# Kernel tuning notes

Measured on AMD Instinct MI355X. Metric: run time of the kernel, lower is better.

Reference implementation:

```python
import jax, jax.numpy as jnp
import numpy as np
from jax import lax

D_MODEL = 1024
D_STATE = 16
D_CONV = 4
EXPAND = 2
D_INNER = EXPAND * D_MODEL
DT_RANK = (D_MODEL + 15) // 16  # ceil(d_model/16) = 64
B, L = 2, 2048
EPS = 1e-5


def setup_inputs() -> dict:
    key = jax.random.key(0)
    ks = jax.random.split(key, 12)
    s = 0.02
    inp = {
        "x": jax.random.normal(ks[0], (B, L, D_MODEL), jnp.float32),
        "ln_g": jnp.ones((D_MODEL,), jnp.float32),
        "ln_b": jnp.zeros((D_MODEL,), jnp.float32),
        "sq_w": jax.random.normal(ks[1], (D_MODEL, D_MODEL), jnp.float32) * s,
        "sq_b": jnp.zeros((D_MODEL,), jnp.float32),
        "srw_w": jax.random.normal(ks[2], (D_MODEL, D_MODEL), jnp.float32) * s,
        "srw_b": jnp.zeros((D_MODEL,), jnp.float32),
        "res_scale": jnp.ones((1,), jnp.float32),
        "in_proj_w": jax.random.normal(ks[3], (D_MODEL, 2 * D_INNER), jnp.float32) * s,
        "conv_w": jax.random.normal(ks[4], (D_INNER, D_CONV), jnp.float32) * 0.1,
        "conv_b": jnp.zeros((D_INNER,), jnp.float32),
        "x_proj_w": jax.random.normal(ks[5], (D_INNER, DT_RANK + 2 * D_STATE), jnp.float32) * s,
        "dt_w": jax.random.normal(ks[6], (DT_RANK, D_INNER), jnp.float32) * s,
        "dt_b": jnp.full((D_INNER,), -4.6, jnp.float32),  # softplus(-4.6)~0.01
        "A_log": jnp.log(jnp.broadcast_to(jnp.arange(1, D_STATE + 1, dtype=jnp.float32), (D_INNER, D_STATE))),
        "D": jnp.ones((D_INNER,), jnp.float32),
        "out_proj_w": jax.random.normal(ks[7], (D_INNER, D_MODEL), jnp.float32) * s,
    }
    return inp


def _layernorm(x, g, b):
    mu = jnp.mean(x, axis=-1, keepdims=True)
    var = jnp.mean(jnp.square(x - mu), axis=-1, keepdims=True)
    return (x - mu) * lax.rsqrt(var + EPS) * g + b


def _causal_dwconv(u, w, b):
    # u: [B,L,Din], w: [Din,d_conv] -> causal depthwise conv
    din, dc = w.shape
    up = jnp.pad(u, ((0, 0), (dc - 1, 0), (0, 0)))
    k = w.T[:, None, :]  # [d_conv, 1, Din]
    out = lax.conv_general_dilated(up, k, (1,), "VALID",
                                   dimension_numbers=("NWC", "WIO", "NWC"),
                                   feature_group_count=din)
    return out + b


def _mamba(h, in_proj_w, conv_w, conv_b, x_proj_w, dt_w, dt_b, A_log, D, out_proj_w):
    xz = h @ in_proj_w                       # [B,L,2*Din]
    u, z = jnp.split(xz, 2, axis=-1)
    u = jax.nn.silu(_causal_dwconv(u, conv_w, conv_b))  # [B,L,Din]
    x_dbl = u @ x_proj_w                     # [B,L,R+2N]
    dt, Bm, Cm = jnp.split(x_dbl, [DT_RANK, DT_RANK + D_STATE], axis=-1)
    delta = jax.nn.softplus(dt @ dt_w + dt_b)            # [B,L,Din]
    A = -jnp.exp(A_log)                                  # [Din,N]
    dA = jnp.exp(jnp.einsum("bld,dn->bldn", delta, A))   # [B,L,Din,N]
    dBu = jnp.einsum("bld,bln,bld->bldn", delta, Bm, u)  # [B,L,Din,N]

    def step(hst, inp):
        dA_t, dBu_t, C_t = inp
        hst = dA_t * hst + dBu_t                         # [B,Din,N]
        y = jnp.einsum("bdn,bn->bd", hst, C_t)
        return hst, y

    h0 = jnp.zeros((u.shape[0], D_INNER, D_STATE), u.dtype)
    _, ys = lax.scan(step, h0, (dA.transpose(1, 0, 2, 3),
                                dBu.transpose(1, 0, 2, 3),
                                Cm.transpose(1, 0, 2)))
    y = ys.transpose(1, 0, 2) + u * D                    # [B,L,Din]
    y = y * jax.nn.silu(z)
    return y @ out_proj_w


def reference(x, ln_g, ln_b, sq_w, sq_b, srw_w, srw_b, res_scale,
              in_proj_w, conv_w, conv_b, x_proj_w, dt_w, dt_b, A_log, D, out_proj_w):
    residual = x
    h = _layernorm(x, ln_g, ln_b)
    h = h + (h @ sq_w + sq_b)                # x + spatial_query(x)
    y = _mamba(h, in_proj_w, conv_w, conv_b, x_proj_w, dt_w, dt_b, A_log, D, out_proj_w)
    y = y * (y @ srw_w + srw_b)              # x * spatial_reweight(x)
    return residual + res_scale * y
```

## Files before the change

kernel.cpp:

```cpp
#include <hip/hip_runtime.h>
#include <math.h>


#define DMODEL 1024
#define DINNER 2048
#define NSTATE 16
#define DTRANK 64
#define BATCH  2
#define SEQ    2048
#define ROWS   (BATCH*SEQ)
#define NC     32
#define TS     (SEQ/NC)
#define LN_EPS 1e-5f

typedef unsigned short u16;
typedef __attribute__((ext_vector_type(8))) short bf16x8;
typedef __attribute__((ext_vector_type(4))) float f32x4;

__device__ __forceinline__ float silu_f(float x) { return x / (1.f + __expf(-x)); }

__device__ __forceinline__ u16 f2bf(float f) {
    union { float f; unsigned u; } v; v.f = f;
    unsigned r = v.u + 0x7fffu + ((v.u >> 16) & 1u);
    return (u16)(r >> 16);
}
__device__ __forceinline__ float bf2f(u16 h) {
    union { unsigned u; float f; } v; v.u = ((unsigned)h) << 16; return v.f;
}

__device__ __forceinline__ void gload_lds16(const u16* g, u16* l) {
    __builtin_amdgcn_global_load_lds(
        (const __attribute__((address_space(1))) unsigned int*)(g),
        (__attribute__((address_space(3))) unsigned int*)(static_cast<void*>(l)),
        16, 0, 0);
}

__device__ __forceinline__ void tr_tile(const float* __restrict__ src,
                                        u16* __restrict__ dst,
                                        int R, int C, int xt, int yt, int tx, int ty)
{
    __shared__ float t[32][33];
    int c0 = xt * 32, r0 = yt * 32;
    #pragma unroll
    for (int i = 0; i < 32; i += 8) {
        float v = 0.f;
        if (c0 + tx < C) v = src[(size_t)(r0 + ty + i) * C + c0 + tx];
        t[ty + i][tx] = v;
    }
    __syncthreads();
    #pragma unroll
    for (int i = 0; i < 32; i += 8)
        dst[(size_t)(c0 + ty + i) * R + r0 + tx] = f2bf(t[tx][ty + i]);
}

__global__ __launch_bounds__(256) void prologue_kernel(
    const float* __restrict__ sq_w,  u16* __restrict__ sqT,
    const float* __restrict__ srw_w, u16* __restrict__ srwT,
    const float* __restrict__ inp,   u16* __restrict__ inpT,
    const float* __restrict__ outp,  u16* __restrict__ outpT,
    const float* __restrict__ xp,    u16* __restrict__ xpT,
    const float* __restrict__ dtw,   u16* __restrict__ dtT,
    const float* __restrict__ x,     const float* __restrict__ ln_g,
    const float* __restrict__ ln_b,
    float* __restrict__ h0, u16* __restrict__ h0bf)
{
    int id = blockIdx.x;
    if (id < 8576) {
        int tx = threadIdx.x & 31, ty = threadIdx.x >> 5;
        if (id < 1024)      { tr_tile(sq_w,  sqT,  1024, 1024, id & 31,  id >> 5, tx, ty); }
        else if (id < 2048) { id -= 1024; tr_tile(srw_w, srwT, 1024, 1024, id & 31,  id >> 5, tx, ty); }
        else if (id < 6144) { id -= 2048; tr_tile(inp,  inpT, 1024, 4096, id & 127, id >> 7, tx, ty); }
        else if (id < 8192) { id -= 6144; tr_tile(outp, outpT,2048, 1024, id & 31,  id >> 5, tx, ty); }
        else if (id < 8448) { id -= 8192; tr_tile(xp,   xpT,  2048,   96, id & 3,   id >> 2, tx, ty); }
        else                { id -= 8448; tr_tile(dtw,  dtT,    64, 2048, id & 63,  id >> 6, tx, ty); }
        return;
    }
    int row = id - 8576;
    const float* xr = x + (size_t)row * DMODEL;
    float4 v = ((const float4*)xr)[threadIdx.x];
    float s  = v.x + v.y + v.z + v.w;
    float ss = v.x*v.x + v.y*v.y + v.z*v.z + v.w*v.w;
    #pragma unroll
    for (int off = 32; off; off >>= 1) { s += __shfl_down(s, off); ss += __shfl_down(ss, off); }
    __shared__ float s_s[4], s_ss[4];
    int lane = threadIdx.x & 63, w = threadIdx.x >> 6;
    if (lane == 0) { s_s[w] = s; s_ss[w] = ss; }
    __syncthreads();
    float ts = 0.f, tss = 0.f;
    #pragma unroll
    for (int i = 0; i < 4; i++) { ts += s_s[i]; tss += s_ss[i]; }
    float mu  = ts / (float)DMODEL;
    float var = tss / (float)DMODEL - mu * mu;
    float rstd = rsqrtf(var + LN_EPS);
    float4 gv = ((const float4*)ln_g)[threadIdx.x];
    float4 bv = ((const float4*)ln_b)[threadIdx.x];
    float4 o;
    o.x = (v.x - mu) * rstd * gv.x + bv.x;
    o.y = (v.y - mu) * rstd * gv.y + bv.y;
    o.z = (v.z - mu) * rstd * gv.z + bv.z;
    o.w = (v.w - mu) * rstd * gv.w + bv.w;
    ((float4*)(h0 + (size_t)row * DMODEL))[threadIdx.x] = o;
    unsigned lo = (unsigned)f2bf(o.x) | ((unsigned)f2bf(o.y) << 16);
    unsigned hi = (unsigned)f2bf(o.z) | ((unsigned)f2bf(o.w) << 16);
    ((uint2*)(h0bf + (size_t)row * DMODEL))[threadIdx.x] = make_uint2(lo, hi);
}

__device__ __forceinline__ void stage128(const u16* __restrict__ A, const u16* __restrict__ Bt,
                                         int m0, int n0, int lda, int ldb, int k0,
                                         u16* As, u16* Bs, int tid)
{
    #pragma unroll
    for (int p = 0; p < 2; p++) {
        int idx = p * 256 + tid;
        int row = idx >> 2, seg = idx & 3;
        int ss = seg ^ ((row >> 1) & 3);
        gload_lds16(A  + (size_t)(m0 + row) * lda + k0 + ss * 8, As + idx * 8);
        gload_lds16(Bt + (size_t)(n0 + row) * ldb + k0 + ss * 8, Bs + idx * 8);
    }
}
__device__ __forceinline__ void stage256(const u16* __restrict__ A, const u16* __restrict__ Bt,
                                         int m0, int n0, int lda, int ldb, int k0,
                                         u16* As, u16* Bs, int tid)
{
    #pragma unroll
    for (int p = 0; p < 2; p++) {
        int idx = p * 512 + tid;
        int row = idx >> 2, seg = idx & 3;
        int ss = seg ^ ((row >> 1) & 3);
        gload_lds16(A  + (size_t)(m0 + row) * lda + k0 + ss * 8, As + idx * 8);
        gload_lds16(Bt + (size_t)(n0 + row) * ldb + k0 + ss * 8, Bs + idx * 8);
    }
}

__device__ __forceinline__ void ph128(int t, int nt,
    const u16* __restrict__ A, const u16* __restrict__ Bt,
    int m0, int n0, int lda, int ldb, int tid, int wr, int wc, int g, int r,
    u16* As, u16* Bs, bf16x8 (&avR)[4], bf16x8 (&avW)[4], f32x4 (&acc)[4][4])
{
    if (t + 1 < nt) {
        asm volatile("s_waitcnt vmcnt(0)" ::: "memory");
        __builtin_amdgcn_s_barrier();
        __builtin_amdgcn_sched_barrier(0);
    }
    bf16x8 bv[4];
    {
        const u16* bc = Bs + (t % 3) * 4096;
        #pragma unroll
        for (int ni = 0; ni < 4; ni++) {
            int brow = wc * 64 + ni * 16 + r;
            bv[ni] = *(const bf16x8*)&bc[brow * 32 + ((g ^ ((brow >> 1) & 3)) << 3)];
        }
    }
    __builtin_amdgcn_sched_barrier(0);
    if (t + 1 < nt) {
        const u16* ac = As + ((t + 1) % 3) * 4096;
        #pragma unroll
        for (int mi = 0; mi < 4; mi++) {
            int arow = wr * 64 + mi * 16 + r;
            avW[mi] = *(const bf16x8*)&ac[arow * 32 + ((g ^ ((arow >> 1) & 3)) << 3)];
        }
    }
    if (t + 2 < nt)
        stage128(A, Bt, m0, n0, lda, ldb, (t + 2) << 5,
                 As + ((t + 2) % 3) * 4096, Bs + ((t + 2) % 3) * 4096, tid);
    if (t + 1 < nt) asm volatile("s_waitcnt lgkmcnt(4)" ::: "memory");
    else            asm volatile("s_waitcnt lgkmcnt(0)" ::: "memory");
    __builtin_amdgcn_sched_barrier(0);
    #pragma unroll
    for (int mi = 0; mi < 4; mi++)
        #pragma unroll
        for (int ni = 0; ni < 4; ni++)
            acc[mi][ni] = __builtin_amdgcn_mfma_f32_16x16x32_bf16(avR[mi], bv[ni], acc[mi][ni], 0, 0, 0);
}

__device__ __forceinline__ void ph256(int t, int nt,
    const u16* __restrict__ A, const u16* __restrict__ Bt,
    int m0, int n0, int lda, int ldb, int tid, int wr, int wc, int g, int r,
    u16* As, u16* Bs, bf16x8 (&avR)[8], bf16x8 (&avW)[8], f32x4 (&acc)[8][4])
{
    if (t + 1 < nt) {
        asm volatile("s_waitcnt vmcnt(0)" ::: "memory");
        __builtin_amdgcn_s_barrier();
        __builtin_amdgcn_sched_barrier(0);
    }
    bf16x8 bv[4];
    {
        const u16* bc = Bs + (t % 3) * 8192;
        #pragma unroll
        for (int ni = 0; ni < 4; ni++) {
            int brow = wc * 64 + ni * 16 + r;
            bv[ni] = *(const bf16x8*)&bc[brow * 32 + ((g ^ ((brow >> 1) & 3)) << 3)];
        }
    }
    __builtin_amdgcn_sched_barrier(0);
    if (t + 1 < nt) {
        const u16* ac = As + ((t + 1) % 3) * 8192;
        #pragma unroll
        for (int mi = 0; mi < 8; mi++) {
            int arow = wr * 128 + mi * 16 + r;
            avW[mi] = *(const bf16x8*)&ac[arow * 32 + ((g ^ ((arow >> 1) & 3)) << 3)];
        }
    }
    if (t + 2 < nt)
        stage256(A, Bt, m0, n0, lda, ldb, (t + 2) << 5,
                 As + ((t + 2) % 3) * 8192, Bs + ((t + 2) % 3) * 8192, tid);
    if (t + 1 < nt) asm volatile("s_waitcnt lgkmcnt(8)" ::: "memory");
    else            asm volatile("s_waitcnt lgkmcnt(0)" ::: "memory");
    __builtin_amdgcn_sched_barrier(0);
    __builtin_amdgcn_s_setprio(1);
    #pragma unroll
    for (int mi = 0; mi < 8; mi++)
        #pragma unroll
        for (int ni = 0; ni < 4; ni++)
            acc[mi][ni] = __builtin_amdgcn_mfma_f32_16x16x32_bf16(avR[mi], bv[ni], acc[mi][ni], 0, 0, 0);
    __builtin_amdgcn_s_setprio(0);
}

template<int ACT, bool HAS_BIAS, bool HAS_RES, bool WRITE_BF16, bool WRITE_F32, bool FUSE_FINAL>
__global__ __launch_bounds__(256) void gemm_bf16(
    const u16* __restrict__ A, const u16* __restrict__ Bt,
    float* __restrict__ C, u16* __restrict__ Cbf,
    const float* __restrict__ bias, const float* __restrict__ res,
    const float* __restrict__ xres, const float* __restrict__ rsp,
    int K, int lda, int ldb, int ldc, int Nout, int splitK)
{
    if (splitK) {
        int sp = blockIdx.z;
        A  += (size_t)sp * splitK;
        Bt += (size_t)sp * splitK;
        C  += (size_t)sp * ROWS * ldc;
        K = splitK;
    }
    __shared__ __align__(16) u16 As[3 * 4096];
    __shared__ __align__(16) u16 Bs[3 * 4096];
    const int tid = threadIdx.x;
    const int wv = tid >> 6, ln = tid & 63;
    const int m0 = blockIdx.y * 128, n0 = blockIdx.x * 128;
    const int g = ln >> 4, r = ln & 15;
    const int wr = wv >> 1, wc = wv & 1;

    f32x4 acc[4][4];
    #pragma unroll
    for (int i = 0; i < 4; i++)
        #pragma unroll
        for (int j = 0; j < 4; j++) acc[i][j] = (f32x4)0.f;

    const int nt = K >> 5;
    stage128(A, Bt, m0, n0, lda, ldb, 0,  As,        Bs,        tid);
    stage128(A, Bt, m0, n0, lda, ldb, 32, As + 4096, Bs + 4096, tid);
    asm volatile("s_waitcnt vmcnt(4)" ::: "memory");
    __builtin_amdgcn_s_barrier();
    __builtin_amdgcn_sched_barrier(0);

    bf16x8 avA[4], avB[4];
    #pragma unroll
    for (int mi = 0; mi < 4; mi++) {
        int arow = wr * 64 + mi * 16 + r;
        avA[mi] = *(const bf16x8*)&As[arow * 32 + ((g ^ ((arow >> 1) & 3)) << 3)];
    }
    for (int tt = 0; tt < nt; tt += 2) {
        ph128(tt,     nt, A, Bt, m0, n0, lda, ldb, tid, wr, wc, g, r, As, Bs, avA, avB, acc);
        ph128(tt + 1, nt, A, Bt, m0, n0, lda, ldb, tid, wr, wc, g, r, As, Bs, avB, avA, acc);
    }

    float rs = FUSE_FINAL ? rsp[0] : 0.f;
    #pragma unroll
    for (int mi = 0; mi < 4; mi++) {
        int row0 = m0 + wr * 64 + mi * 16 + g * 4;
        #pragma unroll
        for (int ni = 0; ni < 4; ni++) {
            int col = n0 + wc * 64 + ni * 16 + r;
            if (col >= Nout) continue;
            float bb = HAS_BIAS ? bias[col] : 0.f;
            #pragma unroll
            for (int j = 0; j < 4; j++) {
                int row = row0 + j;
                float c = acc[mi][ni][j] + bb;
                if (HAS_RES) c += res[(size_t)row * ldc + col];
                if (ACT == 1) c = logf(1.f + __expf(c));
                if (FUSE_FINAL) {
                    float yv = res[(size_t)row * ldc + col];
                    c = xres[(size_t)row * ldc + col] + rs * yv * c;
                }
                if (WRITE_F32 || FUSE_FINAL) C[(size_t)row * ldc + col] = c;
                if (WRITE_BF16) Cbf[(size_t)row * ldc + col] = f2bf(c);
            }
        }
    }
}

template<bool ZSILU>
__global__ __launch_bounds__(512, 2) void gemm256_bf16(
    const u16* __restrict__ A, const u16* __restrict__ Bt, u16* __restrict__ Cbf,
    int K, int lda, int ldb, int ldc)
{
    __shared__ __align__(16) u16 As[3 * 8192];
    __shared__ __align__(16) u16 Bs[3 * 8192];
    const int tid = threadIdx.x;
    const int wv = tid >> 6, ln = tid & 63;
    const int g = ln >> 4, r = ln & 15;
    const int wr = wv >> 2, wc = wv & 3;
    const int m0 = blockIdx.y * 256, n0 = blockIdx.x * 256;

    f32x4 acc[8][4];
    #pragma unroll
    for (int i = 0; i < 8; i++)
        #pragma unroll
        for (int j = 0; j < 4; j++) acc[i][j] = (f32x4)0.f;

    const int nt = K >> 5;
    stage256(A, Bt, m0, n0, lda, ldb, 0,  As,        Bs,        tid);
    stage256(A, Bt, m0, n0, lda, ldb, 32, As + 8192, Bs + 8192, tid);
    asm volatile("s_waitcnt vmcnt(4)" ::: "memory");
    __builtin_amdgcn_s_barrier();
    __builtin_amdgcn_sched_barrier(0);

    bf16x8 avA[8], avB[8];
    #pragma unroll
    for (int mi = 0; mi < 8; mi++) {
        int arow = wr * 128 + mi * 16 + r;
        avA[mi] = *(const bf16x8*)&As[arow * 32 + ((g ^ ((arow >> 1) & 3)) << 3)];
    }
    for (int tt = 0; tt < nt; tt += 2) {
        ph256(tt,     nt, A, Bt, m0, n0, lda, ldb, tid, wr, wc, g, r, As, Bs, avA, avB, acc);
        ph256(tt + 1, nt, A, Bt, m0, n0, lda, ldb, tid, wr, wc, g, r, As, Bs, avB, avA, acc);
    }

    const bool isz = ZSILU && (n0 >= DINNER);
    #pragma unroll
    for (int mi = 0; mi < 8; mi++) {
        int row0 = m0 + wr * 128 + mi * 16 + g * 4;
        #pragma unroll
        for (int ni = 0; ni < 4; ni++) {
            int col = n0 + wc * 64 + ni * 16 + r;
            #pragma unroll
            for (int j = 0; j < 4; j++) {
                float c = acc[mi][ni][j];
                if (isz) c = silu_f(c);
                Cbf[(size_t)(row0 + j) * ldc + col] = f2bf(c);
            }
        }
    }
}

__global__ __launch_bounds__(256) void reduce_xproj(const float* __restrict__ part,
                                                    float* __restrict__ xdbl,
                                                    u16* __restrict__ xdbl_bf)
{
    int i = blockIdx.x * 256 + threadIdx.x;
    const int SL = ROWS * 96;
    float s = 0.f;
    #pragma unroll
    for (int k = 0; k < 8; k++) s += part[i + k * SL];
    xdbl[i] = s;
    xdbl_bf[i] = f2bf(s);
}

__global__ __launch_bounds__(256) void conv_silu_kernel(
    const u16* __restrict__ xzbf, const float* __restrict__ w,
    const float* __restrict__ b, u16* __restrict__ u)
{
    size_t idx = (size_t)blockIdx.x * 256 + threadIdx.x;
    int d = (int)(idx & (DINNER - 1));
    int r = (int)(idx >> 11);
    int t = r & (SEQ - 1);
    float4 wv = *(const float4*)(w + (size_t)d * 4);
    float acc = b[d];
    const float* wf = (const float*)&wv;
    #pragma unroll
    for (int j = 0; j < 4; j++) {
        int tt = t - 3 + j;
        if (tt >= 0)
            acc = fmaf(bf2f(xzbf[(size_t)(r - 3 + j) * 4096 + d]), wf[j], acc);
    }
    u[idx] = f2bf(silu_f(acc));
}

__global__ __launch_bounds__(256) void scan_phaseA(
    const u16* __restrict__ delta,
    const u16* __restrict__ u,
    const float* __restrict__ xdbl,
    const float* __restrict__ A_log,
    float* __restrict__ S, float* __restrict__ sumdlt)
{
    int d = blockIdx.x * 256 + threadIdx.x;
    int c = blockIdx.y, b = blockIdx.z;
    float Ad[NSTATE];
    #pragma unroll
    for (int n = 0; n < NSTATE; n++) Ad[n] = -__expf(A_log[(size_t)d * NSTATE + n]);
    float hs[NSTATE];
    #pragma unroll
    for (int n = 0; n < NSTATE; n++) hs[n] = 0.f;
    float sd = 0.f;
    int r0 = b * SEQ + c * TS;
    for (int t = 0; t < TS; t++) {
        int r = r0 + t;
        float dlt = bf2f(delta[(size_t)r * DINNER + d]);
        float uu  = bf2f(u[(size_t)r * DINNER + d]);
        const float* bm = xdbl + (size_t)r * 96 + DTRANK;
        float du = dlt * uu;
        sd += dlt;
        #pragma unroll
        for (int n = 0; n < NSTATE; n++) {
            float dA = __expf(dlt * Ad[n]);
            hs[n] = fmaf(dA, hs[n], du * bm[n]);
        }
    }
    size_t base = ((size_t)(b * NC + c) * DINNER + d) * NSTATE;
    #pragma unroll
    for (int n = 0; n < NSTATE; n += 4)
        *(float4*)(S + base + n) = make_float4(hs[n], hs[n+1], hs[n+2], hs[n+3]);
    sumdlt[(size_t)(b * NC + c) * DINNER + d] = sd;
}

__global__ __launch_bounds__(256) void scan_phaseB(
    const float* __restrict__ S, const float* __restrict__ sumdlt,
    const float* __restrict__ A_log, float* __restrict__ Hin)
{
    int idx = blockIdx.x * 256 + threadIdx.x;
    int b  = idx >> 15;
    int dn = idx & (DINNER * NSTATE - 1);
    float Ad = -__expf(A_log[dn]);
    int d = dn >> 4;
    const size_t stride = (size_t)DINNER * NSTATE;
    size_t base  = (size_t)b * NC * stride + dn;
    size_t sbase = (size_t)b * NC * DINNER + d;
    float h = 0.f;
    for (int c = 0; c < NC; c++) {
        size_t off = base + (size_t)c * stride;
        float p = __expf(Ad * sumdlt[sbase + (size_t)c * DINNER]);
        float s = S[off];
        Hin[off] = h;
        h = fmaf(p, h, s);
    }
}

__global__ __launch_bounds__(256) void scan_phaseC(
    const u16* __restrict__ delta,
    u16* __restrict__ u,
    const float* __restrict__ xdbl,
    const float* __restrict__ A_log,
    const float* __restrict__ Hin,
    const float* __restrict__ Dp,
    const u16* __restrict__ xzbf)
{
    int d = blockIdx.x * 256 + threadIdx.x;
    int c = blockIdx.y, b = blockIdx.z;
    float Ad[NSTATE];
    #pragma unroll
    for (int n = 0; n < NSTATE; n++) Ad[n] = -__expf(A_log[(size_t)d * NSTATE + n]);
    float hs[NSTATE];
    size_t hbase = ((size_t)(b * NC + c) * DINNER + d) * NSTATE;
    #pragma unroll
    for (int n = 0; n < NSTATE; n++) hs[n] = Hin[hbase + n];
    float Dd = Dp[d];
    int r0 = b * SEQ + c * TS;
    for (int t = 0; t < TS; t++) {
        int r = r0 + t;
        float dlt = bf2f(delta[(size_t)r * DINNER + d]);
        float uu  = bf2f(u[(size_t)r * DINNER + d]);
        const float* bm = xdbl + (size_t)r * 96 + DTRANK;
        const float* cm = bm + NSTATE;
        float du = dlt * uu;
        float y = 0.f;
        #pragma unroll
        for (int n = 0; n < NSTATE; n++) {
            float dA = __expf(dlt * Ad[n]);
            hs[n] = fmaf(dA, hs[n], du * bm[n]);
            y = fmaf(hs[n], cm[n], y);
        }
        float sz = bf2f(xzbf[(size_t)r * 4096 + DINNER + d]);
        u[(size_t)r * DINNER + d] = f2bf((y + uu * Dd) * sz);
    }
}

extern "C" void kernel_launch(void* const* d_in, const int* in_sizes, int n_in,
                              void* d_out, int out_size, void* d_ws, size_t ws_size,
                              hipStream_t stream)
{
    const float* x         = (const float*)d_in[0];
    const float* ln_g      = (const float*)d_in[1];
    const float* ln_b      = (const float*)d_in[2];
    const float* sq_w      = (const float*)d_in[3];
    const float* sq_b      = (const float*)d_in[4];
    const float* srw_w     = (const float*)d_in[5];
    const float* srw_b     = (const float*)d_in[6];
    const float* res_scale = (const float*)d_in[7];
    const float* in_proj_w = (const float*)d_in[8];
    const float* conv_w    = (const float*)d_in[9];
    const float* conv_b    = (const float*)d_in[10];
    const float* x_proj_w  = (const float*)d_in[11];
    const float* dt_w      = (const float*)d_in[12];
    const float* dt_b      = (const float*)d_in[13];
    const float* A_log     = (const float*)d_in[14];
    const float* Dp        = (const float*)d_in[15];
    const float* out_proj_w= (const float*)d_in[16];
    float* out = (float*)d_out;

    char* ws = (char*)d_ws;
    float* h0      = (float*)(ws + 0);
    u16*   delta_bf= (u16*)  (ws + 0);
    float* y2      = (float*)(ws + 0);
    float* xpart   = (float*)(ws + ((size_t)16 << 20));
    u16*   xz_bf   = (u16*)  (ws + ((size_t)32 << 20));
    u16*   u_bf    = (u16*)  (ws + ((size_t)64 << 20));
    float* xdbl    = (float*)(ws + ((size_t)80 << 20));
    u16*   xprojT  = (u16*)  (ws + ((size_t)82 << 20));
    u16*   h0_bf   = (u16*)  (ws + ((size_t)83 << 20));
    u16*   xdbl_bf = (u16*)  (ws + ((size_t)83 << 20));
    u16*   h_bf    = (u16*)  (ws + ((size_t)91 << 20));
    float* sumdlt  = (float*)(ws + ((size_t)91 << 20));
    float* S       = (float*)(ws + ((size_t)99 << 20));
    u16*   y2_bf   = (u16*)  (ws + ((size_t)99 << 20));
    float* Hin     = (float*)(ws + ((size_t)115 << 20));
    u16*   sqT     = (u16*)  (ws + ((size_t)131 << 20));
    u16*   srwT    = (u16*)  (ws + ((size_t)133 << 20));
    u16*   inprojT = (u16*)  (ws + ((size_t)135 << 20));
    u16*   outprojT= (u16*)  (ws + ((size_t)143 << 20));
    u16*   dtT     = (u16*)  (ws + ((size_t)147 << 20));

    dim3 blk(256);

    prologue_kernel<<<8576 + ROWS, blk, 0, stream>>>(
        sq_w, sqT, srw_w, srwT, in_proj_w, inprojT, out_proj_w, outprojT,
        x_proj_w, xprojT, dt_w, dtT, x, ln_g, ln_b, h0, h0_bf);
    gemm_bf16<0, true, true, true, false, false><<<dim3(8, 32), blk, 0, stream>>>(
        h0_bf, sqT, nullptr, h_bf, sq_b, h0, nullptr, nullptr, DMODEL, DMODEL, DMODEL, DMODEL, DMODEL, 0);
    gemm256_bf16<true><<<dim3(16, 16), dim3(512), 0, stream>>>(
        h_bf, inprojT, xz_bf, DMODEL, DMODEL, DMODEL, 2 * DINNER);
    conv_silu_kernel<<<(ROWS * DINNER) / 256, blk, 0, stream>>>(xz_bf, conv_w, conv_b, u_bf);
    gemm_bf16<0, false, false, false, true, false><<<dim3(1, 32, 8), blk, 0, stream>>>(
        u_bf, xprojT, xpart, nullptr, nullptr, nullptr, nullptr, nullptr,
        DINNER, DINNER, DINNER, 96, 96, DINNER / 8);
    reduce_xproj<<<(ROWS * 96) / 256, blk, 0, stream>>>(xpart, xdbl, xdbl_bf);
    gemm_bf16<1, true, false, true, false, false><<<dim3(16, 32), blk, 0, stream>>>(
        xdbl_bf, dtT, nullptr, delta_bf, dt_b, nullptr, nullptr, nullptr,
        DTRANK, 96, DTRANK, DINNER, DINNER, 0);
    scan_phaseA<<<dim3(DINNER / 256, NC, BATCH), blk, 0, stream>>>(delta_bf, u_bf, xdbl, A_log, S, sumdlt);
    scan_phaseB<<<dim3((BATCH * DINNER * NSTATE) / 256), blk, 0, stream>>>(S, sumdlt, A_log, Hin);
    scan_phaseC<<<dim3(DINNER / 256, NC, BATCH), blk, 0, stream>>>(delta_bf, u_bf, xdbl, A_log, Hin, Dp, xz_bf);
    gemm_bf16<0, false, false, true, true, false><<<dim3(8, 32), blk, 0, stream>>>(
        u_bf, outprojT, y2, y2_bf, nullptr, nullptr, nullptr, nullptr,
        DINNER, DINNER, DINNER, DMODEL, DMODEL, 0);
    gemm_bf16<0, true, false, false, false, true><<<dim3(8, 32), blk, 0, stream>>>(
        y2_bf, srwT, out, nullptr, srw_b, y2, x, res_scale,
        DMODEL, DMODEL, DMODEL, DMODEL, DMODEL, 0);
}
```

Measured before the change: 279.0 us.

## Deepen GEMM pipeline, split lgkm waits per column, drop fp32 y2 write

The 256-tile GEMM moves to a 4-stage LDS ring, prefetching three tiles ahead and waiting on vmcnt(4) rather than draining all loads. Both GEMM phases now issue MFMAs column by column behind graded lgkmcnt waits, so compute can start before every LDS read has landed. Separately, the out_proj GEMM no longer writes an fp32 copy of y2, and the final fused GEMM reads the bf16 y2 for its residual multiply. This cuts memory traffic but lowers the precision of that multiply, and the larger LDS footprint may reduce occupancy.

```diff
diff --git a/kernel.cpp b/kernel.cpp
--- a/kernel.cpp
+++ b/kernel.cpp
@@ -34,6 +34,8 @@
         (__attribute__((address_space(3))) unsigned int*)(static_cast<void*>(l)),
         16, 0, 0);
 }
+
+#define SB() __builtin_amdgcn_sched_barrier(0)
 
 __device__ __forceinline__ void tr_tile(const float* __restrict__ src,
                                         u16* __restrict__ dst,
@@ -135,12 +137,13 @@
 __device__ __forceinline__ void ph128(int t, int nt,
     const u16* __restrict__ A, const u16* __restrict__ Bt,
     int m0, int n0, int lda, int ldb, int tid, int wr, int wc, int g, int r,
-    u16* As, u16* Bs, bf16x8 (&avR)[4], bf16x8 (&avW)[4], f32x4 (&acc)[4][4])
-{
-    if (t + 1 < nt) {
+    u16* As, u16* Bs, bf16x8 (&aR)[4], bf16x8 (&aW)[4], f32x4 (&acc)[4][4])
+{
+    const bool haveNext = (t + 1 < nt);
+    if (haveNext) {
         asm volatile("s_waitcnt vmcnt(0)" ::: "memory");
         __builtin_amdgcn_s_barrier();
-        __builtin_amdgcn_sched_barrier(0);
+        SB();
     }
     bf16x8 bv[4];
     {
@@ -151,69 +154,87 @@
             bv[ni] = *(const bf16x8*)&bc[brow * 32 + ((g ^ ((brow >> 1) & 3)) << 3)];
         }
     }
-    __builtin_amdgcn_sched_barrier(0);
-    if (t + 1 < nt) {
+    SB();
+    if (haveNext) {
         const u16* ac = As + ((t + 1) % 3) * 4096;
         #pragma unroll
         for (int mi = 0; mi < 4; mi++) {
             int arow = wr * 64 + mi * 16 + r;
-            avW[mi] = *(const bf16x8*)&ac[arow * 32 + ((g ^ ((arow >> 1) & 3)) << 3)];
-        }
+            aW[mi] = *(const bf16x8*)&ac[arow * 32 + ((g ^ ((arow >> 1) & 3)) << 3)];
+        }
+        SB();
     }
     if (t + 2 < nt)
         stage128(A, Bt, m0, n0, lda, ldb, (t + 2) << 5,
                  As + ((t + 2) % 3) * 4096, Bs + ((t + 2) % 3) * 4096, tid);
-    if (t + 1 < nt) asm volatile("s_waitcnt lgkmcnt(4)" ::: "memory");
-    else            asm volatile("s_waitcnt lgkmcnt(0)" ::: "memory");
-    __builtin_amdgcn_sched_barrier(0);
-    #pragma unroll
-    for (int mi = 0; mi < 4; mi++)
-        #pragma unroll
-        for (int ni = 0; ni < 4; ni++)
-            acc[mi][ni] = __builtin_amdgcn_mfma_f32_16x16x32_bf16(avR[mi], bv[ni], acc[mi][ni], 0, 0, 0);
+#define COL128(ni) { _Pragma("unroll") \
+    for (int mi = 0; mi < 4; mi++) \
+        acc[mi][ni] = __builtin_amdgcn_mfma_f32_16x16x32_bf16(aR[mi], bv[ni], acc[mi][ni], 0, 0, 0); }
+    if (haveNext) {
+        asm volatile("s_waitcnt lgkmcnt(7)" ::: "memory"); SB(); COL128(0);
+        asm volatile("s_waitcnt lgkmcnt(6)" ::: "memory"); SB(); COL128(1);
+        asm volatile("s_waitcnt lgkmcnt(5)" ::: "memory"); SB(); COL128(2);
+        asm volatile("s_waitcnt lgkmcnt(4)" ::: "memory"); SB(); COL128(3);
+    } else {
+        asm volatile("s_waitcnt lgkmcnt(3)" ::: "memory"); SB(); COL128(0);
+        asm volatile("s_waitcnt lgkmcnt(2)" ::: "memory"); SB(); COL128(1);
+        asm volatile("s_waitcnt lgkmcnt(1)" ::: "memory"); SB(); COL128(2);
+        asm volatile("s_waitcnt lgkmcnt(0)" ::: "memory"); SB(); COL128(3);
+    }
+#undef COL128
 }
 
 __device__ __forceinline__ void ph256(int t, int nt,
     const u16* __restrict__ A, const u16* __restrict__ Bt,
     int m0, int n0, int lda, int ldb, int tid, int wr, int wc, int g, int r,
-    u16* As, u16* Bs, bf16x8 (&avR)[8], bf16x8 (&avW)[8], f32x4 (&acc)[8][4])
-{
-    if (t + 1 < nt) {
-        asm volatile("s_waitcnt vmcnt(0)" ::: "memory");
+    u16* As, u16* Bs, bf16x8 (&aR)[8], bf16x8 (&aW)[8], f32x4 (&acc)[8][4])
+{
+    const bool haveNext = (t + 1 < nt);
+    if (haveNext) {
+        if (t + 2 < nt) asm volatile("s_waitcnt vmcnt(4)" ::: "memory");
+        else            asm volatile("s_waitcnt vmcnt(0)" ::: "memory");
         __builtin_amdgcn_s_barrier();
-        __builtin_amdgcn_sched_barrier(0);
+        SB();
     }
     bf16x8 bv[4];
     {
-        const u16* bc = Bs + (t % 3) * 8192;
+        const u16* bc = Bs + (t & 3) * 8192;
         #pragma unroll
         for (int ni = 0; ni < 4; ni++) {
             int brow = wc * 64 + ni * 16 + r;
             bv[ni] = *(const bf16x8*)&bc[brow * 32 + ((g ^ ((brow >> 1) & 3)) << 3)];
         }
     }
-    __builtin_amdgcn_sched_barrier(0);
-    if (t + 1 < nt) {
-        const u16* ac = As + ((t + 1) % 3) * 8192;
+    SB();
+    if (haveNext) {
+        const u16* ac = As + ((t + 1) & 3) * 8192;
         #pragma unroll
         for (int mi = 0; mi < 8; mi++) {
             int arow = wr * 128 + mi * 16 + r;
-            avW[mi] = *(const bf16x8*)&ac[arow * 32 + ((g ^ ((arow >> 1) & 3)) << 3)];
-        }
-    }
-    if (t + 2 < nt)
-        stage256(A, Bt, m0, n0, lda, ldb, (t + 2) << 5,
-                 As + ((t + 2) % 3) * 8192, Bs + ((t + 2) % 3) * 8192, tid);
-    if (t + 1 < nt) asm volatile("s_waitcnt lgkmcnt(8)" ::: "memory");
-    else            asm volatile("s_waitcnt lgkmcnt(0)" ::: "memory");
-    __builtin_amdgcn_sched_barrier(0);
+            aW[mi] = *(const bf16x8*)&ac[arow * 32 + ((g ^ ((arow >> 1) & 3)) << 3)];
+        }
+        SB();
+    }
+    if (t + 3 < nt)
+        stage256(A, Bt, m0, n0, lda, ldb, (t + 3) << 5,
+                 As + ((t + 3) & 3) * 8192, Bs + ((t + 3) & 3) * 8192, tid);
+#define COL256(ni) { _Pragma("unroll") \
+    for (int mi = 0; mi < 8; mi++) \
+        acc[mi][ni] = __builtin_amdgcn_mfma_f32_16x16x32_bf16(aR[mi], bv[ni], acc[mi][ni], 0, 0, 0); }
     __builtin_amdgcn_s_setprio(1);
-    #pragma unroll
-    for (int mi = 0; mi < 8; mi++)
-        #pragma unroll
-        for (int ni = 0; ni < 4; ni++)
-            acc[mi][ni] = __builtin_amdgcn_mfma_f32_16x16x32_bf16(avR[mi], bv[ni], acc[mi][ni], 0, 0, 0);
+    if (haveNext) {
+        asm volatile("s_waitcnt lgkmcnt(11)" ::: "memory"); SB(); COL256(0);
+        asm volatile("s_waitcnt lgkmcnt(10)" ::: "memory"); SB(); COL256(1);
+        asm volatile("s_waitcnt lgkmcnt(9)"  ::: "memory"); SB(); COL256(2);
+        asm volatile("s_waitcnt lgkmcnt(8)"  ::: "memory"); SB(); COL256(3);
+    } else {
+        asm volatile("s_waitcnt lgkmcnt(3)" ::: "memory"); SB(); COL256(0);
+        asm volatile("s_waitcnt lgkmcnt(2)" ::: "memory"); SB(); COL256(1);
+        asm volatile("s_waitcnt lgkmcnt(1)" ::: "memory"); SB(); COL256(2);
+        asm volatile("s_waitcnt lgkmcnt(0)" ::: "memory"); SB(); COL256(3);
+    }
     __builtin_amdgcn_s_setprio(0);
+#undef COL256
 }
 
 template<int ACT, bool HAS_BIAS, bool HAS_RES, bool WRITE_BF16, bool WRITE_F32, bool FUSE_FINAL>
@@ -221,6 +242,7 @@
     const u16* __restrict__ A, const u16* __restrict__ Bt,
     float* __restrict__ C, u16* __restrict__ Cbf,
     const float* __restrict__ bias, const float* __restrict__ res,
+    const u16* __restrict__ resbf,
     const float* __restrict__ xres, const float* __restrict__ rsp,
     int K, int lda, int ldb, int ldc, int Nout, int splitK)
 {
@@ -250,7 +272,7 @@
     stage128(A, Bt, m0, n0, lda, ldb, 32, As + 4096, Bs + 4096, tid);
     asm volatile("s_waitcnt vmcnt(4)" ::: "memory");
     __builtin_amdgcn_s_barrier();
-    __builtin_amdgcn_sched_barrier(0);
+    SB();
 
     bf16x8 avA[4], avB[4];
     #pragma unroll
@@ -258,6 +280,7 @@
         int arow = wr * 64 + mi * 16 + r;
         avA[mi] = *(const bf16x8*)&As[arow * 32 + ((g ^ ((arow >> 1) & 3)) << 3)];
     }
+    SB();
     for (int tt = 0; tt < nt; tt += 2) {
         ph128(tt,     nt, A, Bt, m0, n0, lda, ldb, tid, wr, wc, g, r, As, Bs, avA, avB, acc);
         ph128(tt + 1, nt, A, Bt, m0, n0, lda, ldb, tid, wr, wc, g, r, As, Bs, avB, avA, acc);
@@ -279,7 +302,7 @@
                 if (HAS_RES) c += res[(size_t)row * ldc + col];
                 if (ACT == 1) c = logf(1.f + __expf(c));
                 if (FUSE_FINAL) {
-                    float yv = res[(size_t)row * ldc + col];
+                    float yv = bf2f(resbf[(size_t)row * ldc + col]);
                     c = xres[(size_t)row * ldc + col] + rs * yv * c;
                 }
                 if (WRITE_F32 || FUSE_FINAL) C[(size_t)row * ldc + col] = c;
@@ -294,8 +317,8 @@
     const u16* __restrict__ A, const u16* __restrict__ Bt, u16* __restrict__ Cbf,
     int K, int lda, int ldb, int ldc)
 {
-    __shared__ __align__(16) u16 As[3 * 8192];
-    __shared__ __align__(16) u16 Bs[3 * 8192];
+    __shared__ __align__(16) u16 As[4 * 8192];
+    __shared__ __align__(16) u16 Bs[4 * 8192];
     const int tid = threadIdx.x;
     const int wv = tid >> 6, ln = tid & 63;
     const int g = ln >> 4, r = ln & 15;
@@ -309,11 +332,12 @@
         for (int j = 0; j < 4; j++) acc[i][j] = (f32x4)0.f;
 
     const int nt = K >> 5;
-    stage256(A, Bt, m0, n0, lda, ldb, 0,  As,        Bs,        tid);
-    stage256(A, Bt, m0, n0, lda, ldb, 32, As + 8192, Bs + 8192, tid);
-    asm volatile("s_waitcnt vmcnt(4)" ::: "memory");
+    stage256(A, Bt, m0, n0, lda, ldb, 0,  As,         Bs,         tid);
+    stage256(A, Bt, m0, n0, lda, ldb, 32, As + 8192,  Bs + 8192,  tid);
+    stage256(A, Bt, m0, n0, lda, ldb, 64, As + 16384, Bs + 16384, tid);
+    asm volatile("s_waitcnt vmcnt(8)" ::: "memory");
     __builtin_amdgcn_s_barrier();
-    __builtin_amdgcn_sched_barrier(0);
+    SB();
 
     bf16x8 avA[8], avB[8];
     #pragma unroll
@@ -321,6 +345,7 @@
         int arow = wr * 128 + mi * 16 + r;
         avA[mi] = *(const bf16x8*)&As[arow * 32 + ((g ^ ((arow >> 1) & 3)) << 3)];
     }
+    SB();
     for (int tt = 0; tt < nt; tt += 2) {
         ph256(tt,     nt, A, Bt, m0, n0, lda, ldb, tid, wr, wc, g, r, As, Bs, avA, avB, acc);
         ph256(tt + 1, nt, A, Bt, m0, n0, lda, ldb, tid, wr, wc, g, r, As, Bs, avB, avA, acc);
@@ -500,7 +525,6 @@
     char* ws = (char*)d_ws;
     float* h0      = (float*)(ws + 0);
     u16*   delta_bf= (u16*)  (ws + 0);
-    float* y2      = (float*)(ws + 0);
     float* xpart   = (float*)(ws + ((size_t)16 << 20));
     u16*   xz_bf   = (u16*)  (ws + ((size_t)32 << 20));
     u16*   u_bf    = (u16*)  (ws + ((size_t)64 << 20));
@@ -525,24 +549,25 @@
         sq_w, sqT, srw_w, srwT, in_proj_w, inprojT, out_proj_w, outprojT,
         x_proj_w, xprojT, dt_w, dtT, x, ln_g, ln_b, h0, h0_bf);
     gemm_bf16<0, true, true, true, false, false><<<dim3(8, 32), blk, 0, stream>>>(
-        h0_bf, sqT, nullptr, h_bf, sq_b, h0, nullptr, nullptr, DMODEL, DMODEL, DMODEL, DMODEL, DMODEL, 0);
+        h0_bf, sqT, nullptr, h_bf, sq_b, h0, nullptr, nullptr, nullptr,
+        DMODEL, DMODEL, DMODEL, DMODEL, DMODEL, 0);
     gemm256_bf16<true><<<dim3(16, 16), dim3(512), 0, stream>>>(
         h_bf, inprojT, xz_bf, DMODEL, DMODEL, DMODEL, 2 * DINNER);
     conv_silu_kernel<<<(ROWS * DINNER) / 256, blk, 0, stream>>>(xz_bf, conv_w, conv_b, u_bf);
     gemm_bf16<0, false, false, false, true, false><<<dim3(1, 32, 8), blk, 0, stream>>>(
-        u_bf, xprojT, xpart, nullptr, nullptr, nullptr, nullptr, nullptr,
+        u_bf, xprojT, xpart, nullptr, nullptr, nullptr, nullptr, nullptr, nullptr,
         DINNER, DINNER, DINNER, 96, 96, DINNER / 8);
     reduce_xproj<<<(ROWS * 96) / 256, blk, 0, stream>>>(xpart, xdbl, xdbl_bf);
     gemm_bf16<1, true, false, true, false, false><<<dim3(16, 32), blk, 0, stream>>>(
-        xdbl_bf, dtT, nullptr, delta_bf, dt_b, nullptr, nullptr, nullptr,
+        xdbl_bf, dtT, nullptr, delta_bf, dt_b, nullptr, nullptr, nullptr, nullptr,
         DTRANK, 96, DTRANK, DINNER, DINNER, 0);
     scan_phaseA<<<dim3(DINNER / 256, NC, BATCH), blk, 0, stream>>>(delta_bf, u_bf, xdbl, A_log, S, sumdlt);
     scan_phaseB<<<dim3((BATCH * DINNER * NSTATE) / 256), blk, 0, stream>>>(S, sumdlt, A_log, Hin);
     scan_phaseC<<<dim3(DINNER / 256, NC, BATCH), blk, 0, stream>>>(delta_bf, u_bf, xdbl, A_log, Hin, Dp, xz_bf);
-    gemm_bf16<0, false, false, true, true, false><<<dim3(8, 32), blk, 0, stream>>>(
-        u_bf, outprojT, y2, y2_bf, nullptr, nullptr, nullptr, nullptr,
+    gemm_bf16<0, false, false, true, false, false><<<dim3(8, 32), blk, 0, stream>>>(
+        u_bf, outprojT, nullptr, y2_bf, nullptr, nullptr, nullptr, nullptr, nullptr,
         DINNER, DINNER, DINNER, DMODEL, DMODEL, 0);
     gemm_bf16<0, true, false, false, false, true><<<dim3(8, 32), blk, 0, stream>>>(
-        y2_bf, srwT, out, nullptr, srw_b, y2, x, res_scale,
+        y2_bf, srwT, out, nullptr, srw_b, nullptr, y2_bf, x, res_scale,
         DMODEL, DMODEL, DMODEL, DMODEL, DMODEL, 0);
 }
```

Result: slower. 656.3 us (+135.2%).
